# Kernel tuning notes

Measured on AMD Instinct MI355X. Metric: run time of the kernel, lower is better.

The kernel has to match this reference:

```python
import jax, jax.numpy as jnp
import numpy as np

N_NODES = 10000


def gcn_conv(x, W, b, src, dst, num_nodes):
    """PyG GCNConv: add self-loops, symmetric deg^{-1/2} normalization,
    linear transform (no bias in lin), scatter-add aggregation, then bias."""
    xw = x @ W  # (N, H)
    # degree on A + I (self-loops added)
    deg = jnp.zeros((num_nodes,), dtype=x.dtype).at[dst].add(1.0) + 1.0
    dinv = jax.lax.rsqrt(deg)  # (N,)
    norm = dinv[src] * dinv[dst]  # (E,)
    msg = xw[src] * norm[:, None]  # (E, H) gathered messages
    agg = jax.ops.segment_sum(msg, dst, num_segments=num_nodes)
    # self-loop contribution: norm_ii = dinv_i^2
    agg = agg + xw * (dinv * dinv)[:, None]
    return agg + b


def setup_inputs() -> dict:
    key = jax.random.key(0)
    k1, k2, k3, k4 = jax.random.split(key, 4)
    N, F, H, E = N_NODES, 256, 512, 320000
    x = jax.random.normal(k1, (N, F), dtype=jnp.float32)
    edge_index = jax.random.randint(k2, (2, E), 0, N, dtype=jnp.int64)
    W1 = jax.random.normal(k3, (F, H), dtype=jnp.float32) * (1.0 / np.sqrt(F))
    b1 = jnp.zeros((H,), dtype=jnp.float32)
    W2 = jax.random.normal(k4, (H, F), dtype=jnp.float32) * (1.0 / np.sqrt(H))
    b2 = jnp.zeros((F,), dtype=jnp.float32)
    return {"x": x, "edge_index": edge_index, "W1": W1, "b1": b1, "W2": W2, "b2": b2}


def reference(x, edge_index, W1, b1, W2, b2):
    src, dst = edge_index[0], edge_index[1]
    h = jax.nn.relu(gcn_conv(x, W1, b1, src, dst, N_NODES))
    h = jax.nn.relu(gcn_conv(h, W2, b2, src, dst, N_NODES))
    # global_max_pool with single graph (batch all zeros) -> (1, F)
    return jnp.max(h, axis=0, keepdims=True)
```

## Files before the change

### kernel.cpp

```cpp
#include <hip/hip_runtime.h>

#define NNODES 10000
#define MP 10112
#define F 256
#define H 512
#define CAP 128
#define H1STR 520

typedef _Float16 half8 __attribute__((ext_vector_type(8)));
typedef float floatx4 __attribute__((ext_vector_type(4)));
typedef float floatx8 __attribute__((ext_vector_type(8)));

__global__ __launch_bounds__(256) void prep_k(const float* __restrict__ W1,
                                              const float* __restrict__ W2,
                                              const float* __restrict__ x,
                                              _Float16* __restrict__ W1t,
                                              _Float16* __restrict__ W2t,
                                              _Float16* __restrict__ xh,
                                              int* __restrict__ cnt) {
  int gt = blockIdx.x * 256 + threadIdx.x;
  if (gt < NNODES) cnt[gt] = 0;
  if (gt < H * F) {
    W1t[gt] = (_Float16)W1[(gt & 255) * H + (gt >> 8)];
    W2t[gt] = (_Float16)W2[(gt & 511) * F + (gt >> 9)];
  }
  if (gt < NNODES * F / 8) {
    floatx8 v = *(const floatx8*)(x + (size_t)gt * 8);
    *(half8*)(xh + (size_t)gt * 8) = __builtin_convertvector(v, half8);
  }
}

__global__ __launch_bounds__(256) void build_k(const int* __restrict__ src,
                                               const int* __restrict__ dst,
                                               int* __restrict__ cnt,
                                               int* __restrict__ csr, int E) {
  int e = blockIdx.x * blockDim.x + threadIdx.x;
  if (e < E) {
    int d = dst[e];
    int p = atomicAdd(&cnt[d], 1);
    if (p < CAP) csr[(size_t)d * CAP + p] = src[e];
  }
}

template <bool FUSE_MAX>
__global__ __launch_bounds__(256) void aggb_k(const _Float16* __restrict__ in,
                                              const int* __restrict__ cnt,
                                              const int* __restrict__ csr,
                                              const float* __restrict__ bias,
                                              _Float16* __restrict__ outh,
                                              float* __restrict__ out) {
  __shared__ float smem[2048];
  int tid = threadIdx.x;
  int lane = tid & 63, wvi = tid >> 6;
  int half = lane >> 5, hl = lane & 31;
  int f0 = hl * 8;
  int node = (blockIdx.x * 4 + wvi) * 2 + half;
  floatx8 bb = {};
  if (FUSE_MAX) bb = *(const floatx8*)(bias + f0);
  floatx8 lmax = {};
  {
    int deg = min(cnt[node], CAP);
    float di = rsqrtf((float)(deg + 1));
    const int* bucket = csr + (size_t)node * CAP;
    floatx8 acc = {};
    for (int c = 0; c < deg; c += 32) {
      int mm = min(32, deg - c);
      int sv = 0; float wvv = 0.f;
      if (hl < mm) {
        sv = bucket[c + hl];
        wvv = rsqrtf((float)(cnt[sv] + 1));
      }
      #pragma unroll
      for (int b = 0; b < 2; b++) {
        int base = b * 16;
        if (base < mm) {
          int sj[16]; float wj[16];
          #pragma unroll
          for (int u = 0; u < 16; u++) {
            int l = (half << 5) | (base + u);
            sj[u] = __shfl(sv, l, 64);
            wj[u] = __shfl(wvv, l, 64);
          }
          half8 hv[16];
          #pragma unroll
          for (int u = 0; u < 16; u++)
            hv[u] = *(const half8*)(in + (size_t)sj[u] * F + f0);
          #pragma unroll
          for (int u = 0; u < 16; u++)
            acc += wj[u] * __builtin_convertvector(hv[u], floatx8);
        }
      }
    }
    half8 xsv = *(const half8*)(in + (size_t)node * F + f0);
    floatx8 tot = di * acc + (di * di) * __builtin_convertvector(xsv, floatx8);
    if (FUSE_MAX) {
      tot += bb;
      #pragma unroll
      for (int t = 0; t < 8; t++) lmax[t] = fmaxf(lmax[t], fmaxf(tot[t], 0.f));
    } else {
      *(half8*)(outh + (size_t)node * F + f0) = __builtin_convertvector(tot, half8);
    }
  }
  if (FUSE_MAX) {
    float* srow = smem + (size_t)(wvi * 2 + half) * 256;
    *(floatx8*)(srow + f0) = lmax;
    __syncthreads();
    float m = smem[tid];
    #pragma unroll
    for (int r = 1; r < 8; r++) m = fmaxf(m, smem[r * 256 + tid]);
    atomicMax((int*)&out[tid], __float_as_int(m));
  }
}

__global__ __launch_bounds__(256) void gemm12_k(const _Float16* __restrict__ A,
                                                const _Float16* __restrict__ W1t,
                                                const float* __restrict__ b1,
                                                const _Float16* __restrict__ W2t,
                                                _Float16* __restrict__ C) {
  __shared__ _Float16 h1[32 * H1STR];
  int lane = threadIdx.x & 63;
  int wv = threadIdx.x >> 6;
  int r = lane & 15, q = lane >> 4;
  int m0 = blockIdx.x * 32;

  {
    floatx4 acc[2][8] = {};
    const _Float16* Ap = A + (size_t)(m0 + r) * F + q * 8;
    const _Float16* Bp = W1t + (size_t)(wv * 128 + r) * F + q * 8;
    for (int k0 = 0; k0 < F; k0 += 32) {
      half8 a[2], b[8];
      #pragma unroll
      for (int i = 0; i < 2; i++) a[i] = *(const half8*)(Ap + (size_t)i * 16 * F + k0);
      #pragma unroll
      for (int j = 0; j < 8; j++) b[j] = *(const half8*)(Bp + (size_t)j * 16 * F + k0);
      #pragma unroll
      for (int i = 0; i < 2; i++)
        #pragma unroll
        for (int j = 0; j < 8; j++)
          acc[i][j] = __builtin_amdgcn_mfma_f32_16x16x32_f16(a[i], b[j], acc[i][j], 0, 0, 0);
    }
    #pragma unroll
    for (int i = 0; i < 2; i++) {
      #pragma unroll
      for (int j = 0; j < 8; j++) {
        int n = wv * 128 + j * 16 + r;
        float bv = b1[n];
        #pragma unroll
        for (int rr = 0; rr < 4; rr++) {
          int row = i * 16 + q * 4 + rr;
          h1[row * H1STR + n] = (_Float16)fmaxf(acc[i][j][rr] + bv, 0.f);
        }
      }
    }
  }
  __syncthreads();

  {
    floatx4 acc[2][4] = {};
    const _Float16* Bp = W2t + (size_t)(wv * 64 + r) * H + q * 8;
    for (int k0 = 0; k0 < H; k0 += 32) {
      half8 a[2], b[4];
      #pragma unroll
      for (int i = 0; i < 2; i++)
        a[i] = *(const half8*)(h1 + (i * 16 + r) * H1STR + k0 + q * 8);
      #pragma unroll
      for (int j = 0; j < 4; j++) b[j] = *(const half8*)(Bp + (size_t)j * 16 * H + k0);
      #pragma unroll
      for (int i = 0; i < 2; i++)
        #pragma unroll
        for (int j = 0; j < 4; j++)
          acc[i][j] = __builtin_amdgcn_mfma_f32_16x16x32_f16(a[i], b[j], acc[i][j], 0, 0, 0);
    }
    #pragma unroll
    for (int i = 0; i < 2; i++) {
      #pragma unroll
      for (int j = 0; j < 4; j++) {
        int n = wv * 64 + j * 16 + r;
        #pragma unroll
        for (int rr = 0; rr < 4; rr++) {
          int row = m0 + i * 16 + q * 4 + rr;
          C[(size_t)row * F + n] = (_Float16)acc[i][j][rr];
        }
      }
    }
  }
}

extern "C" void kernel_launch(void* const* d_in, const int* in_sizes, int n_in,
                              void* d_out, int out_size, void* d_ws, size_t ws_size,
                              hipStream_t stream) {
  const float* x  = (const float*)d_in[0];
  const int*   ei = (const int*)d_in[1];
  const float* W1 = (const float*)d_in[2];
  const float* b1 = (const float*)d_in[3];
  const float* W2 = (const float*)d_in[4];
  const float* b2 = (const float*)d_in[5];
  const int E = in_sizes[1] / 2;
  const int N = NNODES;
  const int* src = ei;
  const int* dst = ei + E;

  char* w = (char*)d_ws;
  size_t off = 0;
  auto take = [&](size_t bytes) -> void* {
    void* p = w + off;
    off += (bytes + 255) & ~(size_t)255;
    return p;
  };
  int*       cnt    = (int*)take((size_t)N * 4);
  int*       csr    = (int*)take((size_t)N * CAP * 4);
  _Float16*  W1t    = (_Float16*)take((size_t)H * F * 2);
  _Float16*  W2t    = (_Float16*)take((size_t)F * H * 2);
  _Float16*  xh     = (_Float16*)take((size_t)N * F * 2);
  _Float16*  axh    = (_Float16*)take((size_t)MP * F * 2);
  _Float16*  xw2h   = (_Float16*)take((size_t)MP * F * 2);

  prep_k<<<1250, 256, 0, stream>>>(W1, W2, x, W1t, W2t, xh, cnt);
  build_k<<<(E + 255) / 256, 256, 0, stream>>>(src, dst, cnt, csr, E);
  aggb_k<false><<<1250, 256, 0, stream>>>(xh, cnt, csr, nullptr, axh, nullptr);
  gemm12_k<<<MP / 32, 256, 0, stream>>>(axh, W1t, b1, W2t, xw2h);
  aggb_k<true><<<1250, 256, 0, stream>>>(xw2h, cnt, csr, b2, nullptr, (float*)d_out);
}
```

Baseline: 178.6 us.

## Pre-scale features by source dinv so aggregation needs no per-edge weights

Folds the source-side deg^{-1/2} factor into the feature rows before aggregation: x is scaled in prep (now run after CSR build), and the layer-2 GEMM output is scaled by dinv per row. The gather loop then only sums rows plus the self row, dropping the per-edge cnt lookup, rsqrt and weight shuffles. A zero padding row replaces bounds handling, and the next chunk of neighbour indices is prefetched. This costs an extra kernel launch and puts prep on the critical path after build_k.

```diff
diff --git a/kernel.cpp b/kernel.cpp
--- a/kernel.cpp
+++ b/kernel.cpp
@@ -6,28 +6,15 @@
 #define H 512
 #define CAP 128
 #define H1STR 520
+#define ZROW NNODES
 
 typedef _Float16 half8 __attribute__((ext_vector_type(8)));
 typedef float floatx4 __attribute__((ext_vector_type(4)));
 typedef float floatx8 __attribute__((ext_vector_type(8)));
 
-__global__ __launch_bounds__(256) void prep_k(const float* __restrict__ W1,
-                                              const float* __restrict__ W2,
-                                              const float* __restrict__ x,
-                                              _Float16* __restrict__ W1t,
-                                              _Float16* __restrict__ W2t,
-                                              _Float16* __restrict__ xh,
-                                              int* __restrict__ cnt) {
+__global__ __launch_bounds__(256) void zero_k(int* __restrict__ cnt) {
   int gt = blockIdx.x * 256 + threadIdx.x;
   if (gt < NNODES) cnt[gt] = 0;
-  if (gt < H * F) {
-    W1t[gt] = (_Float16)W1[(gt & 255) * H + (gt >> 8)];
-    W2t[gt] = (_Float16)W2[(gt & 511) * F + (gt >> 9)];
-  }
-  if (gt < NNODES * F / 8) {
-    floatx8 v = *(const floatx8*)(x + (size_t)gt * 8);
-    *(half8*)(xh + (size_t)gt * 8) = __builtin_convertvector(v, half8);
-  }
 }
 
 __global__ __launch_bounds__(256) void build_k(const int* __restrict__ src,
@@ -39,6 +26,34 @@
     int d = dst[e];
     int p = atomicAdd(&cnt[d], 1);
     if (p < CAP) csr[(size_t)d * CAP + p] = src[e];
+  }
+}
+
+__global__ __launch_bounds__(256) void prep_k(const float* __restrict__ W1,
+                                              const float* __restrict__ W2,
+                                              const float* __restrict__ x,
+                                              const int* __restrict__ cnt,
+                                              _Float16* __restrict__ W1t,
+                                              _Float16* __restrict__ W2t,
+                                              _Float16* __restrict__ xh,
+                                              float* __restrict__ dinv) {
+  int gt = blockIdx.x * 256 + threadIdx.x;
+  if (gt < NNODES) dinv[gt] = rsqrtf((float)(cnt[gt] + 1));
+  if (gt < H * F) {
+    W1t[gt] = (_Float16)W1[(gt & 255) * H + (gt >> 8)];
+    W2t[gt] = (_Float16)W2[(gt & 511) * F + (gt >> 9)];
+  }
+  if (gt < NNODES * F / 8) {
+    int row = gt >> 5;
+    float di = rsqrtf((float)(cnt[row] + 1));
+    floatx8 v = *(const floatx8*)(x + (size_t)gt * 8);
+    #pragma unroll
+    for (int t = 0; t < 8; t++) v[t] *= di;
+    *(half8*)(xh + (size_t)gt * 8) = __builtin_convertvector(v, half8);
+  }
+  if (gt < F / 8) {
+    half8 z = {};
+    *(half8*)(xh + (size_t)ZROW * F + (size_t)gt * 8) = z;
   }
 }
 
@@ -55,53 +70,55 @@
   int half = lane >> 5, hl = lane & 31;
   int f0 = hl * 8;
   int node = (blockIdx.x * 4 + wvi) * 2 + half;
+  float one = 1.0f;
+  asm("" : "+v"(one));
   floatx8 bb = {};
   if (FUSE_MAX) bb = *(const floatx8*)(bias + f0);
-  floatx8 lmax = {};
-  {
-    int deg = min(cnt[node], CAP);
-    float di = rsqrtf((float)(deg + 1));
-    const int* bucket = csr + (size_t)node * CAP;
-    floatx8 acc = {};
-    for (int c = 0; c < deg; c += 32) {
-      int mm = min(32, deg - c);
-      int sv = 0; float wvv = 0.f;
-      if (hl < mm) {
-        sv = bucket[c + hl];
-        wvv = rsqrtf((float)(cnt[sv] + 1));
-      }
-      #pragma unroll
-      for (int b = 0; b < 2; b++) {
-        int base = b * 16;
-        if (base < mm) {
-          int sj[16]; float wj[16];
+
+  int degfull = cnt[node];
+  int deg = min(degfull, CAP);
+  float di = rsqrtf((float)(degfull + 1));
+  const int* bucket = csr + (size_t)node * CAP;
+  const _Float16* inf = in + f0;
+
+  half8 xsv = *(const half8*)(inf + (size_t)node * F);
+  int sv = ZROW;
+  if (hl < deg) sv = bucket[hl];
+
+  floatx8 acc;
+  #pragma unroll
+  for (int t = 0; t < 8; t++) acc[t] = (float)xsv[t];
+
+  for (int c = 0; c < deg; c += 32) {
+    int mm = min(32, deg - c);
+    int svn = ZROW;
+    int rem = deg - c - 32;
+    if (hl < rem) svn = bucket[c + 32 + hl];
+    #pragma unroll
+    for (int b = 0; b < 2; b++) {
+      int base = b * 16;
+      if (base < mm) {
+        int sj[16];
+        #pragma unroll
+        for (int u = 0; u < 16; u++) sj[u] = __shfl(sv, (half << 5) | (base + u), 64);
+        half8 hv[16];
+        #pragma unroll
+        for (int u = 0; u < 16; u++)
+          hv[u] = *(const half8*)(inf + (size_t)sj[u] * F);
+        #pragma unroll
+        for (int u = 0; u < 16; u++)
           #pragma unroll
-          for (int u = 0; u < 16; u++) {
-            int l = (half << 5) | (base + u);
-            sj[u] = __shfl(sv, l, 64);
-            wj[u] = __shfl(wvv, l, 64);
-          }
-          half8 hv[16];
-          #pragma unroll
-          for (int u = 0; u < 16; u++)
-            hv[u] = *(const half8*)(in + (size_t)sj[u] * F + f0);
-          #pragma unroll
-          for (int u = 0; u < 16; u++)
-            acc += wj[u] * __builtin_convertvector(hv[u], floatx8);
-        }
-      }
-    }
-    half8 xsv = *(const half8*)(in + (size_t)node * F + f0);
-    floatx8 tot = di * acc + (di * di) * __builtin_convertvector(xsv, floatx8);
-    if (FUSE_MAX) {
-      tot += bb;
-      #pragma unroll
-      for (int t = 0; t < 8; t++) lmax[t] = fmaxf(lmax[t], fmaxf(tot[t], 0.f));
-    } else {
-      *(half8*)(outh + (size_t)node * F + f0) = __builtin_convertvector(tot, half8);
-    }
-  }
+          for (int t = 0; t < 8; t++)
+            acc[t] = __builtin_fmaf((float)hv[u][t], one, acc[t]);
+      }
+    }
+    sv = svn;
+  }
+
   if (FUSE_MAX) {
+    floatx8 lmax;
+    #pragma unroll
+    for (int t = 0; t < 8; t++) lmax[t] = fmaxf(di * acc[t] + bb[t], 0.f);
     float* srow = smem + (size_t)(wvi * 2 + half) * 256;
     *(floatx8*)(srow + f0) = lmax;
     __syncthreads();
@@ -109,6 +126,11 @@
     #pragma unroll
     for (int r = 1; r < 8; r++) m = fmaxf(m, smem[r * 256 + tid]);
     atomicMax((int*)&out[tid], __float_as_int(m));
+  } else {
+    floatx8 tot;
+    #pragma unroll
+    for (int t = 0; t < 8; t++) tot[t] = di * acc[t];
+    *(half8*)(outh + (size_t)node * F + f0) = __builtin_convertvector(tot, half8);
   }
 }
 
@@ -116,6 +138,7 @@
                                                 const _Float16* __restrict__ W1t,
                                                 const float* __restrict__ b1,
                                                 const _Float16* __restrict__ W2t,
+                                                const float* __restrict__ dinv,
                                                 _Float16* __restrict__ C) {
   __shared__ _Float16 h1[32 * H1STR];
   int lane = threadIdx.x & 63;
@@ -156,6 +179,14 @@
   __syncthreads();
 
   {
+    float sc[2][4];
+    #pragma unroll
+    for (int i = 0; i < 2; i++)
+      #pragma unroll
+      for (int rr = 0; rr < 4; rr++) {
+        int row = m0 + i * 16 + q * 4 + rr;
+        sc[i][rr] = (row < NNODES) ? dinv[row] : 0.f;
+      }
     floatx4 acc[2][4] = {};
     const _Float16* Bp = W2t + (size_t)(wv * 64 + r) * H + q * 8;
     for (int k0 = 0; k0 < H; k0 += 32) {
@@ -179,7 +210,8 @@
         #pragma unroll
         for (int rr = 0; rr < 4; rr++) {
           int row = m0 + i * 16 + q * 4 + rr;
-          C[(size_t)row * F + n] = (_Float16)acc[i][j][rr];
+          float val = (row < NNODES) ? acc[i][j][rr] * sc[i][rr] : 0.f;
+          C[(size_t)row * F + n] = (_Float16)val;
         }
       }
     }
@@ -211,13 +243,15 @@
   int*       csr    = (int*)take((size_t)N * CAP * 4);
   _Float16*  W1t    = (_Float16*)take((size_t)H * F * 2);
   _Float16*  W2t    = (_Float16*)take((size_t)F * H * 2);
-  _Float16*  xh     = (_Float16*)take((size_t)N * F * 2);
+  _Float16*  xh     = (_Float16*)take((size_t)(N + 1) * F * 2);
+  float*     dinvp  = (float*)take((size_t)N * 4);
   _Float16*  axh    = (_Float16*)take((size_t)MP * F * 2);
   _Float16*  xw2h   = (_Float16*)take((size_t)MP * F * 2);
 
-  prep_k<<<1250, 256, 0, stream>>>(W1, W2, x, W1t, W2t, xh, cnt);
+  zero_k<<<(N + 255) / 256, 256, 0, stream>>>(cnt);
   build_k<<<(E + 255) / 256, 256, 0, stream>>>(src, dst, cnt, csr, E);
+  prep_k<<<1250, 256, 0, stream>>>(W1, W2, x, cnt, W1t, W2t, xh, dinvp);
   aggb_k<false><<<1250, 256, 0, stream>>>(xh, cnt, csr, nullptr, axh, nullptr);
-  gemm12_k<<<MP / 32, 256, 0, stream>>>(axh, W1t, b1, W2t, xw2h);
+  gemm12_k<<<MP / 32, 256, 0, stream>>>(axh, W1t, b1, W2t, dinvp, xw2h);
   aggb_k<true><<<1250, 256, 0, stream>>>(xw2h, cnt, csr, b2, nullptr, (float*)d_out);
 }
```

New measurement: 180.4 us. About the same (+1.0%).
